# Kernel optimization log

Hardware: AMD Instinct MI355X
Metric: run time of the kernel (lower is better)

Reference implementation:

```python
import jax, jax.numpy as jnp
import numpy as np
import math

THETA = 10000.0
NUM_HEADS = 16


def apply_rope(x, pos, theta):
    # x: [B, H, S, Dh], pos: [S]
    d_k = x.shape[-1]
    inv_freq = theta ** (-jnp.arange(0, d_k, 2, dtype=x.dtype) / d_k)  # [Dh/2]
    angles = pos.astype(x.dtype)[:, None] * inv_freq  # [S, Dh/2]
    cos = jnp.cos(angles)
    sin = jnp.sin(angles)
    x_even = x[..., ::2]
    x_odd = x[..., 1::2]
    out_even = x_even * cos - x_odd * sin
    out_odd = x_even * sin + x_odd * cos
    # interleave back: stack on trailing axis then flatten
    return jnp.stack((out_even, out_odd), axis=-1).reshape(x.shape)


def setup_inputs() -> dict:
    key = jax.random.key(0)
    ks = jax.random.split(key, 5)
    B, S, D = 2, 2048, 1024
    scale = 1.0 / math.sqrt(D)
    return {
        "in_features": jax.random.normal(ks[0], (B, S, D), dtype=jnp.float32),
        "token_positions": jnp.arange(S, dtype=jnp.int64 if jax.config.jax_enable_x64 else jnp.int32),
        "Wq": jax.random.normal(ks[1], (D, D), dtype=jnp.float32) * scale,
        "Wk": jax.random.normal(ks[2], (D, D), dtype=jnp.float32) * scale,
        "Wv": jax.random.normal(ks[3], (D, D), dtype=jnp.float32) * scale,
        "Wo": jax.random.normal(ks[4], (D, D), dtype=jnp.float32) * scale,
    }


def reference(in_features, token_positions, Wq, Wk, Wv, Wo):
    B, S, D = in_features.shape
    H = NUM_HEADS
    Dh = D // H

    def split_heads(x):  # [B,S,D] -> [B,H,S,Dh]
        return x.reshape(B, S, H, Dh).transpose(0, 2, 1, 3)

    # nn.Linear convention: y = x @ W.T
    q = split_heads(in_features @ Wq.T)
    k = split_heads(in_features @ Wk.T)
    v = split_heads(in_features @ Wv.T)

    q = apply_rope(q, token_positions, THETA)
    k = apply_rope(k, token_positions, THETA)

    scores = jnp.einsum('bhqd,bhkd->bhqk', q, k) / jnp.sqrt(jnp.asarray(Dh, q.dtype))
    causal = jnp.tril(jnp.ones((S, S), dtype=bool))
    scores = jnp.where(causal, scores, jnp.asarray(-jnp.inf, scores.dtype))
    weights = jax.nn.softmax(scores, axis=-1)
    out = jnp.einsum('bhqk,bhkd->bhqd', weights, v)  # [B,H,S,Dh]
    out = out.transpose(0, 2, 1, 3).reshape(B, S, D)
    return out @ Wo.T
```

## Files before the change

kernel.cpp:

```cpp
#include <hip/hip_runtime.h>
#include <hip/hip_bf16.h>


typedef __bf16 bf16x8 __attribute__((ext_vector_type(8)));
typedef float floatx4 __attribute__((ext_vector_type(4)));
typedef float floatx16 __attribute__((ext_vector_type(16)));
typedef int intx2 __attribute__((ext_vector_type(2)));

#define MFMA16(A, B, C) __builtin_amdgcn_mfma_f32_16x16x32_bf16((A), (B), (C), 0, 0, 0)
#define MFMA32(A, B, C) __builtin_amdgcn_mfma_f32_32x32x16_bf16((A), (B), (C), 0, 0, 0)

#define S_LEN 2048
#define D_MODEL 1024
#define NHEAD 16
#define DHEAD 64
#define NTOK 4096
#define NEG_SENTINEL (-1.0e30f)
#define QSCALE_LOG2E 0.18033688011112042f

__device__ __forceinline__ short b16(float f) {
  __bf16 h = (__bf16)f;
  union { __bf16 b; short s; } u; u.b = h;
  return u.s;
}
__device__ __forceinline__ unsigned pk2(float x, float y) {
  union { __bf16 b[2]; unsigned u; } t;
  t.b[0] = (__bf16)x; t.b[1] = (__bf16)y;
  return t.u;
}
__device__ __forceinline__ bf16x8 ld_frag(const short* p) {
  return *(const bf16x8*)p;
}
__device__ __forceinline__ void gl2lds16(const short* g, short* l) {
  __builtin_amdgcn_global_load_lds(
      (const __attribute__((address_space(1))) unsigned int*)g,
      (__attribute__((address_space(3))) unsigned int*)l, 16, 0, 0);
}

__global__ __launch_bounds__(256) void prep_kernel(
    const float* __restrict__ x, const float* __restrict__ wq,
    const float* __restrict__ wk, const float* __restrict__ wv,
    short* __restrict__ xb, short* __restrict__ wqb,
    short* __restrict__ wkb, short* __restrict__ wvb,
    float2* __restrict__ tab) {
  const int y = blockIdx.y;
  if (y == 4) {
    int i = blockIdx.x * 256 + threadIdx.x;
    int s = i >> 5, p = i & 31;
    float inv_freq = __expf(-0.28782313662425575f * (float)p);
    float ang = (float)s * inv_freq;
    float sn, c;
    sincosf(ang, &sn, &c);
    tab[i] = make_float2(c, sn);
    return;
  }
  const float* src = (y == 0) ? x : (y == 1) ? wq : (y == 2) ? wk : wv;
  short* dst = (y == 0) ? xb : (y == 1) ? wqb : (y == 2) ? wkb : wvb;
  const int n4 = ((y == 0) ? NTOK * D_MODEL : D_MODEL * D_MODEL) >> 2;
  for (int i = blockIdx.x * 256 + threadIdx.x; i < n4; i += gridDim.x * 256) {
    float4 v = ((const float4*)src)[i];
    short4 o;
    o.x = b16(v.x); o.y = b16(v.y); o.z = b16(v.z); o.w = b16(v.w);
    ((short4*)dst)[i] = o;
  }
}
__global__ __launch_bounds__(256) void cvt1_kernel(
    const float* __restrict__ src, short* __restrict__ dst, int n4) {
  for (int i = blockIdx.x * 256 + threadIdx.x; i < n4; i += gridDim.x * 256) {
    float4 v = ((const float4*)src)[i];
    short4 o;
    o.x = b16(v.x); o.y = b16(v.y); o.z = b16(v.z); o.w = b16(v.w);
    ((short4*)dst)[i] = o;
  }
}

__global__ __launch_bounds__(256) void qkv_rope_kernel(
    const short* __restrict__ xb,
    const short* __restrict__ Wqb, const short* __restrict__ Wkb,
    const short* __restrict__ Wvb,
    const float2* __restrict__ ropetab,
    short* __restrict__ qws, short* __restrict__ kws, short* __restrict__ vtws) {
  __shared__ __align__(16) short SM[4 * 64 * 72];
  short* As = SM;
  short* Bs = SM + 128 * 32;

  const int tid = threadIdx.x;
  const int lane = tid & 63;
  const int wv = tid >> 6;
  const int col = lane & 15, quad = lane >> 4;
  const int half = lane >> 5, l31 = lane & 31;
  const int wr = wv >> 1, wc = wv & 1;
  const int gemm = blockIdx.y;
  const int bm = blockIdx.x >> 3;
  const int bn = blockIdx.x & 7;
  const short* W = (gemm == 0) ? Wqb : (gemm == 1) ? Wkb : Wvb;

  const int srow = wv * 16 + (lane >> 2);
  const int skoff = (lane & 3) * 8;
  const short* gA0 = xb + (size_t)(bm * 128 + srow) * D_MODEL + skoff;
  const short* gA1 = gA0 + (size_t)64 * D_MODEL;
  const short* gB0 = W + (size_t)(bn * 128 + srow) * D_MODEL + skoff;
  const short* gB1 = gB0 + (size_t)64 * D_MODEL;
  short* lA0 = As + (wv * 16) * 32;
  short* lA1 = lA0 + 64 * 32;
  short* lB0 = Bs + (wv * 16) * 32;
  short* lB1 = lB0 + 64 * 32;

  floatx4 acc[4][4];
#pragma unroll
  for (int i = 0; i < 4; ++i)
#pragma unroll
    for (int j = 0; j < 4; ++j) acc[i][j] = (floatx4){0.f, 0.f, 0.f, 0.f};

  for (int k0 = 0; k0 < D_MODEL; k0 += 32) {
    __syncthreads();
    gl2lds16(gA0 + k0, lA0);
    gl2lds16(gA1 + k0, lA1);
    gl2lds16(gB0 + k0, lB0);
    gl2lds16(gB1 + k0, lB1);
    __syncthreads();
    bf16x8 a[4], b[4];
#pragma unroll
    for (int mt = 0; mt < 4; ++mt)
      a[mt] = ld_frag(&As[(wr * 64 + mt * 16 + col) * 32 + quad * 8]);
#pragma unroll
    for (int nt = 0; nt < 4; ++nt)
      b[nt] = ld_frag(&Bs[(wc * 64 + nt * 16 + col) * 32 + quad * 8]);
#pragma unroll
    for (int mt = 0; mt < 4; ++mt)
#pragma unroll
      for (int nt = 0; nt < 4; ++nt)
        acc[mt][nt] = MFMA16(a[mt], b[nt], acc[mt][nt]);
  }
  __syncthreads();

  const int tm = bm * 2 + wr;
  const int tn = bn * 2 + wc;
  short* Ep = &SM[wv * 64 * 72];
  const int mbase = tm * 64;
  const int bb = mbase >> 11;
  const int s0 = mbase & (S_LEN - 1);

  if (gemm == 2) {
#pragma unroll
    for (int mt = 0; mt < 4; ++mt)
#pragma unroll
      for (int nt = 0; nt < 4; ++nt) {
        int nl = nt * 16 + col;
#pragma unroll
        for (int r = 0; r < 4; ++r)
          Ep[nl * 72 + mt * 16 + quad * 4 + r] = b16(acc[mt][nt][r]);
      }
    short* vb2 = vtws + (size_t)(bb * NHEAD + tn) * S_LEN * DHEAD;
    const int vtile = s0 >> 6;
#pragma unroll
    for (int dt = 0; dt < 2; ++dt) {
      const int4* src = (const int4*)&Ep[(dt * 32 + l31) * 72];
      int4* dst = (int4*)(vb2 + (size_t)(vtile * 8 + dt) * 512);
#pragma unroll
      for (int kc = 0; kc < 4; ++kc)
        dst[kc * 2 * 64 + lane] = src[kc * 2 + half];
    }
  } else {
    short* outp = (gemm == 0) ? qws : kws;
    const float qscale = (gemm == 0) ? QSCALE_LOG2E : 1.0f;
#pragma unroll
    for (int nt = 0; nt < 4; ++nt) {
      int nl = nt * 16 + col;
      const float2* tp = ropetab + (nl >> 1);
#pragma unroll
      for (int mt = 0; mt < 4; ++mt)
#pragma unroll
        for (int r = 0; r < 4; ++r) {
          int ml = mt * 16 + quad * 4 + r;
          float2 cs = tp[(size_t)(s0 + ml) * 32];
          float val = acc[mt][nt][r];
          float partner = __shfl_xor(val, 1);
          float o = ((nl & 1) == 0) ? (val * cs.x - partner * cs.y)
                                    : (partner * cs.y + val * cs.x);
          Ep[ml * 72 + nl] = b16(o * qscale);
        }
    }
    short* ob2 = outp + (size_t)(bb * NHEAD + tn) * S_LEN * DHEAD;
    const int kgrp0 = s0 >> 5;
#pragma unroll
    for (int g2 = 0; g2 < 2; ++g2) {
      const int4* src = (const int4*)&Ep[(g2 * 32 + l31) * 72];
      int4* dst = (int4*)(ob2 + (size_t)((kgrp0 + g2) * 4) * 512);
#pragma unroll
      for (int kc = 0; kc < 4; ++kc)
        dst[kc * 64 + lane] = src[kc * 2 + half];
    }
  }
}

__global__ __launch_bounds__(256) void attn_kernel(
    const short* __restrict__ qws, const short* __restrict__ kws,
    const short* __restrict__ vtws, short* __restrict__ att) {
  const int tid = threadIdx.x;
  const int wv = tid >> 6;
  const int lane = tid & 63;
  const int half = lane >> 5, l31 = lane & 31;
  const int bh = blockIdx.x & 31;
  const int b = bh >> 4, h = bh & 15;
  const int qt = 63 - (blockIdx.x >> 5);
  const int q0 = qt * 32;

  __shared__ float ml[2][4][32];
  __shared__ float Obuf[64][33];

  const short* qbase = qws + (size_t)(b * NHEAD + h) * S_LEN * DHEAD;
  const short* kbase = kws + (size_t)(b * NHEAD + h) * S_LEN * DHEAD;
  const short* vbase = vtws + (size_t)(b * NHEAD + h) * S_LEN * DHEAD;

  bf16x8 qf[4];
#pragma unroll
  for (int kc = 0; kc < 4; ++kc)
    qf[kc] = ld_frag(qbase + (size_t)(qt * 4 + kc) * 512 + lane * 8);

  float m_i = NEG_SENTINEL, l_i = 0.f;
  floatx16 ot[2] = {};

  const int nit = (q0 + 32 + 63) >> 6;

  bf16x8 kfA[2][4];
  auto loadK = [&](int tkt) {
#pragma unroll
    for (int s = 0; s < 2; ++s) {
      if (tkt + s * 32 <= q0 + 31) {
        const short* kr = kbase + (size_t)(((tkt >> 5) + s) * 4) * 512 + lane * 8;
#pragma unroll
        for (int kc = 0; kc < 4; ++kc) kfA[s][kc] = ld_frag(kr + kc * 512);
      }
    }
  };

  int it = wv;
  if (it < nit) loadK(it * 64);

  for (; it < nit; it += 4) {
    const int kt = it * 64;
    bf16x8 vf[4][2];
    {
      const short* vr = vbase + (size_t)(kt >> 6) * 8 * 512 + lane * 8;
#pragma unroll
      for (int kc = 0; kc < 4; ++kc)
#pragma unroll
        for (int dt = 0; dt < 2; ++dt)
          vf[kc][dt] = ld_frag(vr + (size_t)(kc * 2 + dt) * 512);
    }
    floatx16 sc[2];
#pragma unroll
    for (int s = 0; s < 2; ++s) {
      if (kt + s * 32 <= q0 + 31) {
        floatx16 a = {};
#pragma unroll
        for (int kc = 0; kc < 4; ++kc) a = MFMA32(kfA[s][kc], qf[kc], a);
        sc[s] = a;
      } else {
#pragma unroll
        for (int rg = 0; rg < 16; ++rg) sc[s][rg] = NEG_SENTINEL;
      }
    }
    if (it + 4 < nit) loadK((it + 4) * 64);

    if (kt + 63 > q0) {
      const int lim = q0 + l31 - kt;
#pragma unroll
      for (int s = 0; s < 2; ++s)
#pragma unroll
        for (int rg = 0; rg < 16; ++rg) {
          int rel = s * 32 + (rg & 3) + 8 * (rg >> 2) + 4 * half;
          if (rel > lim) sc[s][rg] = NEG_SENTINEL;
        }
    }
    float tr[16];
#pragma unroll
    for (int i = 0; i < 16; ++i) tr[i] = fmaxf(sc[0][i], sc[1][i]);
#pragma unroll
    for (int off = 8; off; off >>= 1)
#pragma unroll
      for (int i = 0; i < off; ++i) tr[i] = fmaxf(tr[i], tr[i + off]);
    float rm = fmaxf(tr[0], __shfl_xor(tr[0], 32));

    if (!__all(rm <= m_i + 8.0f)) {
      float mnew = fmaxf(m_i, rm);
      float alpha = exp2f(m_i - mnew);
      m_i = mnew;
      l_i *= alpha;
#pragma unroll
      for (int dt = 0; dt < 2; ++dt)
#pragma unroll
        for (int rg = 0; rg < 16; ++rg) ot[dt][rg] *= alpha;
    }

    unsigned pw[8][2];
    float rsp[8];
#pragma unroll
    for (int s = 0; s < 2; ++s)
#pragma unroll
      for (int g = 0; g < 4; ++g) {
        float p0 = exp2f(sc[s][4 * g + 0] - m_i);
        float p1 = exp2f(sc[s][4 * g + 1] - m_i);
        float p2 = exp2f(sc[s][4 * g + 2] - m_i);
        float p3 = exp2f(sc[s][4 * g + 3] - m_i);
        rsp[s * 4 + g] = (p0 + p1) + (p2 + p3);
        pw[s * 4 + g][0] = pk2(p0, p1);
        pw[s * 4 + g][1] = pk2(p2, p3);
      }
    float rs = ((rsp[0] + rsp[1]) + (rsp[2] + rsp[3])) +
               ((rsp[4] + rsp[5]) + (rsp[6] + rsp[7]));
    rs += __shfl_xor(rs, 32);
    l_i += rs;

#pragma unroll
    for (int kc = 0; kc < 4; ++kc) {
      intx2 s01 = __builtin_amdgcn_permlane32_swap(
          (int)pw[2 * kc][0], (int)pw[2 * kc + 1][0], false, false);
      intx2 s23 = __builtin_amdgcn_permlane32_swap(
          (int)pw[2 * kc][1], (int)pw[2 * kc + 1][1], false, false);
      union { unsigned u[4]; bf16x8 f; } fr;
      fr.u[0] = (unsigned)s01[0]; fr.u[1] = (unsigned)s23[0];
      fr.u[2] = (unsigned)s01[1]; fr.u[3] = (unsigned)s23[1];
#pragma unroll
      for (int dt = 0; dt < 2; ++dt)
        ot[dt] = MFMA32(vf[kc][dt], fr.f, ot[dt]);
    }
  }

  ml[0][wv][l31] = m_i;
  ml[1][wv][l31] = l_i;
  __syncthreads();
  float m0 = ml[0][0][l31], m1 = ml[0][1][l31];
  float m2 = ml[0][2][l31], m3 = ml[0][3][l31];
  float mtot = fmaxf(fmaxf(m0, m1), fmaxf(m2, m3));
  float sw = exp2f(m_i - mtot);

  if (wv == 0) {
#pragma unroll
    for (int dt = 0; dt < 2; ++dt)
#pragma unroll
      for (int rg = 0; rg < 16; ++rg) {
        int d = dt * 32 + (rg & 3) + 8 * (rg >> 2) + 4 * half;
        Obuf[d][l31] = ot[dt][rg] * sw;
      }
  }
  __syncthreads();
#pragma unroll
  for (int w = 1; w < 4; ++w) {
    if (wv == w) {
#pragma unroll
      for (int dt = 0; dt < 2; ++dt)
#pragma unroll
        for (int rg = 0; rg < 16; ++rg) {
          int d = dt * 32 + (rg & 3) + 8 * (rg >> 2) + 4 * half;
          Obuf[d][l31] += ot[dt][rg] * sw;
        }
    }
    __syncthreads();
  }

  const int q = tid >> 3;
  const int d0 = (tid & 7) * 8;
  float mm0 = ml[0][0][q], mm1 = ml[0][1][q], mm2 = ml[0][2][q], mm3 = ml[0][3][q];
  float mt2 = fmaxf(fmaxf(mm0, mm1), fmaxf(mm2, mm3));
  float lt = ml[1][0][q] * exp2f(mm0 - mt2) + ml[1][1][q] * exp2f(mm1 - mt2) +
             ml[1][2][q] * exp2f(mm2 - mt2) + ml[1][3][q] * exp2f(mm3 - mt2);
  float inv = 1.0f / lt;
  union { bf16x8 hh; int4 i4; } cv;
#pragma unroll
  for (int i = 0; i < 8; ++i) cv.hh[i] = (__bf16)(Obuf[d0 + i][q] * inv);
  int4* dst = (int4*)(att + (size_t)(b * S_LEN + q0 + q) * D_MODEL + h * DHEAD + d0);
  *dst = cv.i4;
}

__global__ __launch_bounds__(256) void out_gemm_kernel(
    const short* __restrict__ att, const short* __restrict__ Wob,
    float* __restrict__ out) {
  __shared__ __align__(16) short As[128 * 32];
  __shared__ __align__(16) short Bs[64 * 32];

  const int tid = threadIdx.x;
  const int lane = tid & 63;
  const int wv = tid >> 6;
  const int col = lane & 15, quad = lane >> 4;
  const int wr = wv >> 1, wc = wv & 1;
  const int bm = blockIdx.x >> 4;
  const int bn = blockIdx.x & 15;

  const int srow = wv * 16 + (lane >> 2);
  const int skoff = (lane & 3) * 8;
  const short* gA0 = att + (size_t)(bm * 128 + srow) * D_MODEL + skoff;
  const short* gA1 = gA0 + (size_t)64 * D_MODEL;
  const short* gB0 = Wob + (size_t)(bn * 64 + srow) * D_MODEL + skoff;
  short* lA0 = As + (wv * 16) * 32;
  short* lA1 = lA0 + 64 * 32;
  short* lB0 = Bs + (wv * 16) * 32;

  floatx4 acc[4][2];
#pragma unroll
  for (int i = 0; i < 4; ++i)
#pragma unroll
    for (int j = 0; j < 2; ++j) acc[i][j] = (floatx4){0.f, 0.f, 0.f, 0.f};

  for (int k0 = 0; k0 < D_MODEL; k0 += 32) {
    __syncthreads();
    gl2lds16(gA0 + k0, lA0);
    gl2lds16(gA1 + k0, lA1);
    gl2lds16(gB0 + k0, lB0);
    __syncthreads();
    bf16x8 a[4], b[2];
#pragma unroll
    for (int mt = 0; mt < 4; ++mt)
      a[mt] = ld_frag(&As[(wr * 64 + mt * 16 + col) * 32 + quad * 8]);
#pragma unroll
    for (int nt = 0; nt < 2; ++nt)
      b[nt] = ld_frag(&Bs[(wc * 32 + nt * 16 + col) * 32 + quad * 8]);
#pragma unroll
    for (int mt = 0; mt < 4; ++mt)
#pragma unroll
      for (int nt = 0; nt < 2; ++nt)
        acc[mt][nt] = MFMA16(a[mt], b[nt], acc[mt][nt]);
  }

#pragma unroll
  for (int mt = 0; mt < 4; ++mt)
#pragma unroll
    for (int nt = 0; nt < 2; ++nt) {
      int n = bn * 64 + wc * 32 + nt * 16 + col;
#pragma unroll
      for (int r = 0; r < 4; ++r) {
        int m = bm * 128 + wr * 64 + mt * 16 + quad * 4 + r;
        out[(size_t)m * D_MODEL + n] = acc[mt][nt][r];
      }
    }
}

extern "C" void kernel_launch(void* const* d_in, const int* in_sizes, int n_in,
                              void* d_out, int out_size, void* d_ws, size_t ws_size,
                              hipStream_t stream) {
  const float* x  = (const float*)d_in[0];
  const float* Wq = (const float*)d_in[2];
  const float* Wk = (const float*)d_in[3];
  const float* Wv = (const float*)d_in[4];
  const float* Wo = (const float*)d_in[5];
  float* out = (float*)d_out;

  const size_t TENS = (size_t)NTOK * D_MODEL;
  const size_t WELEM = (size_t)D_MODEL * D_MODEL;

  short* qws  = (short*)d_out;
  short* xb   = (short*)d_out + TENS;
  short* kws  = (short*)d_ws;
  short* vtws = kws + TENS;
  short* attws = vtws + TENS;
  short* wqb = attws;
  short* wkb = wqb + WELEM;
  short* wvb = wkb + WELEM;
  float2* ropetab = (float2*)(wvb + WELEM);
  short* wob = kws;

  prep_kernel<<<dim3(256, 5), 256, 0, stream>>>(x, Wq, Wk, Wv, xb, wqb, wkb, wvb, ropetab);
  qkv_rope_kernel<<<dim3(256, 3), 256, 0, stream>>>(xb, wqb, wkb, wvb, ropetab, qws, kws, vtws);
  attn_kernel<<<dim3(2048), 256, 0, stream>>>(qws, kws, vtws, attws);
  cvt1_kernel<<<dim3(256), 256, 0, stream>>>(Wo, wob, (int)(WELEM >> 2));
  out_gemm_kernel<<<dim3(512), 256, 0, stream>>>(attws, wob, out);
}
```

Before: 205.1 us.

## Double QKV GEMM K-tile with XOR-swizzled LDS and fuse Wo conversion into out GEMM

The QKV projection GEMM now loads a 64-wide K slice per iteration into an XOR-swizzled shared-memory layout, halving the number of barrier pairs and reducing LDS bank conflicts on fragment reads. Separately, the standalone Wo fp32-to-bf16 conversion kernel is removed and the output GEMM reads fp32 Wo directly, converting to bf16 while staging into LDS. This saves a kernel launch and a round trip of the converted weights. In exchange, each output-GEMM block re-converts Wo tiles redundantly, and the fp32 reads double the B-operand global traffic.

After: 199.1 us. 2.9% less time.

```diff
diff --git a/kernel.cpp b/kernel.cpp
--- a/kernel.cpp
+++ b/kernel.cpp
@@ -64,15 +64,6 @@
     ((short4*)dst)[i] = o;
   }
 }
-__global__ __launch_bounds__(256) void cvt1_kernel(
-    const float* __restrict__ src, short* __restrict__ dst, int n4) {
-  for (int i = blockIdx.x * 256 + threadIdx.x; i < n4; i += gridDim.x * 256) {
-    float4 v = ((const float4*)src)[i];
-    short4 o;
-    o.x = b16(v.x); o.y = b16(v.y); o.z = b16(v.z); o.w = b16(v.w);
-    ((short4*)dst)[i] = o;
-  }
-}
 
 __global__ __launch_bounds__(256) void qkv_rope_kernel(
     const short* __restrict__ xb,
@@ -82,7 +73,7 @@
     short* __restrict__ qws, short* __restrict__ kws, short* __restrict__ vtws) {
   __shared__ __align__(16) short SM[4 * 64 * 72];
   short* As = SM;
-  short* Bs = SM + 128 * 32;
+  short* Bs = SM + 128 * 64;
 
   const int tid = threadIdx.x;
   const int lane = tid & 63;
@@ -95,16 +86,21 @@
   const int bn = blockIdx.x & 7;
   const short* W = (gemm == 0) ? Wqb : (gemm == 1) ? Wkb : Wvb;
 
-  const int srow = wv * 16 + (lane >> 2);
-  const int skoff = (lane & 3) * 8;
-  const short* gA0 = xb + (size_t)(bm * 128 + srow) * D_MODEL + skoff;
-  const short* gA1 = gA0 + (size_t)64 * D_MODEL;
-  const short* gB0 = W + (size_t)(bn * 128 + srow) * D_MODEL + skoff;
-  const short* gB1 = gB0 + (size_t)64 * D_MODEL;
-  short* lA0 = As + (wv * 16) * 32;
-  short* lA1 = lA0 + 64 * 32;
-  short* lB0 = Bs + (wv * 16) * 32;
-  short* lB1 = lB0 + 64 * 32;
+  const int srow8 = lane >> 3;
+  const int scolsw = ((lane & 7) ^ srow8) * 8;
+  const short* gAa[4]; short* lAa[4];
+  const short* gBa[4]; short* lBa[4];
+#pragma unroll
+  for (int g = 0; g < 2; ++g)
+#pragma unroll
+    for (int j = 0; j < 2; ++j) {
+      const int idx = g * 2 + j;
+      const int r0 = g * 64 + wv * 16 + j * 8;
+      gAa[idx] = xb + (size_t)(bm * 128 + r0 + srow8) * D_MODEL + scolsw;
+      lAa[idx] = As + r0 * 64;
+      gBa[idx] = W + (size_t)(bn * 128 + r0 + srow8) * D_MODEL + scolsw;
+      lBa[idx] = Bs + r0 * 64;
+    }
 
   floatx4 acc[4][4];
 #pragma unroll
@@ -112,25 +108,32 @@
 #pragma unroll
     for (int j = 0; j < 4; ++j) acc[i][j] = (floatx4){0.f, 0.f, 0.f, 0.f};
 
-  for (int k0 = 0; k0 < D_MODEL; k0 += 32) {
+  const int arow = wr * 64;
+  const int brow = wc * 64;
+
+  for (int k0 = 0; k0 < D_MODEL; k0 += 64) {
     __syncthreads();
-    gl2lds16(gA0 + k0, lA0);
-    gl2lds16(gA1 + k0, lA1);
-    gl2lds16(gB0 + k0, lB0);
-    gl2lds16(gB1 + k0, lB1);
+#pragma unroll
+    for (int i = 0; i < 4; ++i) gl2lds16(gAa[i] + k0, lAa[i]);
+#pragma unroll
+    for (int i = 0; i < 4; ++i) gl2lds16(gBa[i] + k0, lBa[i]);
     __syncthreads();
-    bf16x8 a[4], b[4];
-#pragma unroll
-    for (int mt = 0; mt < 4; ++mt)
-      a[mt] = ld_frag(&As[(wr * 64 + mt * 16 + col) * 32 + quad * 8]);
-#pragma unroll
-    for (int nt = 0; nt < 4; ++nt)
-      b[nt] = ld_frag(&Bs[(wc * 64 + nt * 16 + col) * 32 + quad * 8]);
-#pragma unroll
-    for (int mt = 0; mt < 4; ++mt)
+#pragma unroll
+    for (int kk = 0; kk < 2; ++kk) {
+      bf16x8 a[4], b[4];
+      const int usel = (kk * 4 + quad) ^ (col & 7);
+#pragma unroll
+      for (int mt = 0; mt < 4; ++mt)
+        a[mt] = ld_frag(&As[(arow + mt * 16 + col) * 64 + usel * 8]);
 #pragma unroll
       for (int nt = 0; nt < 4; ++nt)
-        acc[mt][nt] = MFMA16(a[mt], b[nt], acc[mt][nt]);
+        b[nt] = ld_frag(&Bs[(brow + nt * 16 + col) * 64 + usel * 8]);
+#pragma unroll
+      for (int mt = 0; mt < 4; ++mt)
+#pragma unroll
+        for (int nt = 0; nt < 4; ++nt)
+          acc[mt][nt] = MFMA16(a[mt], b[nt], acc[mt][nt]);
+    }
   }
   __syncthreads();
 
@@ -375,7 +378,7 @@
 }
 
 __global__ __launch_bounds__(256) void out_gemm_kernel(
-    const short* __restrict__ att, const short* __restrict__ Wob,
+    const short* __restrict__ att, const float* __restrict__ Wo,
     float* __restrict__ out) {
   __shared__ __align__(16) short As[128 * 32];
   __shared__ __align__(16) short Bs[64 * 32];
@@ -392,10 +395,13 @@
   const int skoff = (lane & 3) * 8;
   const short* gA0 = att + (size_t)(bm * 128 + srow) * D_MODEL + skoff;
   const short* gA1 = gA0 + (size_t)64 * D_MODEL;
-  const short* gB0 = Wob + (size_t)(bn * 64 + srow) * D_MODEL + skoff;
   short* lA0 = As + (wv * 16) * 32;
   short* lA1 = lA0 + 64 * 32;
-  short* lB0 = Bs + (wv * 16) * 32;
+
+  const int browB = tid >> 2;
+  const int bc8 = (tid & 3) * 8;
+  const float* gBf = Wo + (size_t)(bn * 64 + browB) * D_MODEL + bc8;
+  short* lBw = Bs + browB * 32 + bc8;
 
   floatx4 acc[4][2];
 #pragma unroll
@@ -404,10 +410,15 @@
     for (int j = 0; j < 2; ++j) acc[i][j] = (floatx4){0.f, 0.f, 0.f, 0.f};
 
   for (int k0 = 0; k0 < D_MODEL; k0 += 32) {
+    float4 w0 = *(const float4*)(gBf + k0);
+    float4 w1 = *(const float4*)(gBf + k0 + 4);
     __syncthreads();
     gl2lds16(gA0 + k0, lA0);
     gl2lds16(gA1 + k0, lA1);
-    gl2lds16(gB0 + k0, lB0);
+    union { unsigned u[4]; int4 i4; } bw;
+    bw.u[0] = pk2(w0.x, w0.y); bw.u[1] = pk2(w0.z, w0.w);
+    bw.u[2] = pk2(w1.x, w1.y); bw.u[3] = pk2(w1.z, w1.w);
+    *(int4*)lBw = bw.i4;
     __syncthreads();
     bf16x8 a[4], b[2];
 #pragma unroll
@@ -458,11 +469,9 @@
   short* wkb = wqb + WELEM;
   short* wvb = wkb + WELEM;
   float2* ropetab = (float2*)(wvb + WELEM);
-  short* wob = kws;
 
   prep_kernel<<<dim3(256, 5), 256, 0, stream>>>(x, Wq, Wk, Wv, xb, wqb, wkb, wvb, ropetab);
   qkv_rope_kernel<<<dim3(256, 3), 256, 0, stream>>>(xb, wqb, wkb, wvb, ropetab, qws, kws, vtws);
   attn_kernel<<<dim3(2048), 256, 0, stream>>>(qws, kws, vtws, attws);
-  cvt1_kernel<<<dim3(256), 256, 0, stream>>>(Wo, wob, (int)(WELEM >> 2));
-  out_gemm_kernel<<<dim3(512), 256, 0, stream>>>(attws, wob, out);
-}
+  out_gemm_kernel<<<dim3(512), 256, 0, stream>>>(attws, Wo, out);
+}
```
